# Kernel optimization log

Hardware: AMD Instinct MI355X
Metric: run time of the kernel (lower is better)

Reference implementation:

```python
import jax, jax.numpy as jnp
import numpy as np
import math

N, L, D = 1024, 32, 768
N_OUT, IN_DIM, OUT_DIM = 16, 64, 64
EPS = 1e-8


def setup_inputs() -> dict:
    key = jax.random.key(0)
    ks = jax.random.split(key, 4)
    x = jax.random.normal(ks[0], (N, L, D), jnp.float32)
    mask = jnp.ones((N, L), jnp.float32)
    scaled = lambda k, shape, fan: jax.random.normal(k, shape, jnp.float32) * (1.0 / np.sqrt(fan).astype(np.float32))
    Wscore = scaled(ks[1], (L, D, 1), D)
    Bscore = jnp.zeros((L, 1, 1), jnp.float32)
    Wcap = scaled(ks[2], (L, D, IN_DIM), D)
    Bcap = jnp.zeros((L, 1, IN_DIM), jnp.float32)
    Wvote = scaled(ks[3], (L, N_OUT, IN_DIM, OUT_DIM), IN_DIM)
    Bvote = jnp.zeros((L, N_OUT, 1, OUT_DIM), jnp.float32)
    beta_use = jnp.zeros((L, 1, 1, 1), jnp.float32)
    beta_ign = jnp.zeros((1, N_OUT, 1, 1), jnp.float32)
    return dict(x=x, mask=mask, Wscore=Wscore, Bscore=Bscore, Wcap=Wcap,
                Bcap=Bcap, Wvote=Wvote, Bvote=Bvote, beta_use=beta_use,
                beta_ign=beta_ign, iters=3)


def reference(x, mask, Wscore, Bscore, Wcap, Bcap, Wvote, Bvote, beta_use, beta_ign, iters):
    n_out = Wvote.shape[1]
    half_pi = np.float32(0.5 * math.pi)
    x_t = jnp.transpose(x, (1, 0, 2))                      # [L, N, D]
    a_in = jnp.matmul(x_t, Wscore) + Bscore                # [L, N, 1]
    mu_in = jax.nn.gelu(jnp.matmul(x_t, Wcap) + Bcap, approximate=False)  # [L, N, in_dim]
    f_a_in = jax.nn.sigmoid(a_in) * jnp.transpose(mask)[..., None]        # [L, N, 1]
    f_a_in = f_a_in[:, None, :, :]                         # [L, 1, N, 1]
    # votes: [L, n_out, N, out_dim] (einsum avoids materializing repeated mu_in)
    V = jnp.einsum('lni,lkio->lkno', mu_in, Wvote) + Bvote

    R = jnp.full((1, n_out, 1, 1), 1.0 / n_out, dtype=x.dtype)
    a_out = mu_out = var_out = None
    for t in range(iters):
        if t > 0:
            log_p = (-jnp.sum((V - mu_out[None]) ** 2 / (2.0 * var_out[None] + EPS), axis=-1)
                     - 1.0 - half_pi
                     - 0.5 * jnp.sum(jnp.log(var_out[None] + EPS), axis=-1))   # [L, n_out, N]
            R = jax.nn.softmax(jax.nn.log_sigmoid(a_out)[None] + log_p[..., None], axis=1)
        D_use = f_a_in * R                                  # [L, n_out, N, 1]
        D_ign = f_a_in - D_use
        a_out = jnp.sum(beta_use * D_use, axis=0) - jnp.sum(beta_ign * D_ign, axis=0)  # [n_out, N, 1]
        denom = jnp.sum(D_use, axis=0) + EPS                # [n_out, N, 1]
        mu_out = jnp.sum(D_use * V, axis=0) / denom         # [n_out, N, out_dim]
        var_out = jnp.sum(D_use * (V - mu_out[None]) ** 2, axis=0) / denom

    a_fin = jnp.transpose(a_out[..., 0])                    # [N, n_out]
    mu_fin = jnp.transpose(mu_out, (1, 0, 2))               # [N, n_out, out_dim]
    return a_fin, mu_fin
```

## Files before the change

### kernel.cpp

```cpp
#include <hip/hip_runtime.h>
#include <hip/hip_bf16.h>

#define L_DIM 32
#define N_DIM 1024
#define D_DIM 768
#define K_DIM 16
#define I_DIM 64
#define O_DIM 64
#define EPSF 1e-8f
#define PX 72

typedef unsigned short u16;
typedef __attribute__((ext_vector_type(8))) short short8;
typedef __attribute__((ext_vector_type(4))) float f32x4;
#define MFMA __builtin_amdgcn_mfma_f32_16x16x32_bf16

__device__ __forceinline__ float bf2f(u16 v) {
    union { unsigned int u; float f; } x; x.u = ((unsigned int)v) << 16; return x.f;
}
__device__ __forceinline__ u16 f2bf(float f) {
    union { float f; unsigned int u; } x; x.f = f;
    unsigned int u = x.u;
    u += 0x7FFFu + ((u >> 16) & 1u);
    return (u16)(u >> 16);
}
__device__ __forceinline__ void split2(float v, u16& h, u16& l) {
    u16 hh = f2bf(v);
    h = hh;
    l = f2bf(v - bf2f(hh));
}

__global__ __launch_bounds__(256) void prep_wcap(
    const float* __restrict__ W, u16* __restrict__ H, u16* __restrict__ Lo)
{
    const int l = blockIdx.y, d0 = blockIdx.x * 64, t = threadIdx.x;
    __shared__ float tile[64][65];
    #pragma unroll
    for (int p = 0; p < 4; p++) {
        int dd = p * 16 + (t >> 4), i4 = (t & 15) * 4;
        float4 v = *(const float4*)&W[((size_t)l * D_DIM + d0 + dd) * I_DIM + i4];
        tile[dd][i4] = v.x; tile[dd][i4+1] = v.y; tile[dd][i4+2] = v.z; tile[dd][i4+3] = v.w;
    }
    __syncthreads();
    #pragma unroll
    for (int p = 0; p < 4; p++) {
        int i = p * 16 + (t >> 4), dd0 = (t & 15) * 4;
        u16 h[4], lo[4];
        #pragma unroll
        for (int j = 0; j < 4; j++) split2(tile[dd0 + j][i], h[j], lo[j]);
        size_t base = ((size_t)l * I_DIM + i) * D_DIM + d0 + dd0;
        uint2 ph; ph.x = h[0] | ((unsigned)h[1] << 16); ph.y = h[2] | ((unsigned)h[3] << 16);
        uint2 pl; pl.x = lo[0] | ((unsigned)lo[1] << 16); pl.y = lo[2] | ((unsigned)lo[3] << 16);
        *(uint2*)&H[base] = ph;
        *(uint2*)&Lo[base] = pl;
    }
}

__global__ __launch_bounds__(256) void prep_wvote(
    const float* __restrict__ W, u16* __restrict__ H, u16* __restrict__ Lo)
{
    const int l = blockIdx.y, k = blockIdx.x, t = threadIdx.x;
    __shared__ float tile[64][65];
    #pragma unroll
    for (int p = 0; p < 4; p++) {
        int i = p * 16 + (t >> 4), o4 = (t & 15) * 4;
        float4 v = *(const float4*)&W[(((size_t)l * K_DIM + k) * I_DIM + i) * O_DIM + o4];
        tile[i][o4] = v.x; tile[i][o4+1] = v.y; tile[i][o4+2] = v.z; tile[i][o4+3] = v.w;
    }
    __syncthreads();
    #pragma unroll
    for (int p = 0; p < 4; p++) {
        int o = p * 16 + (t >> 4), i0 = (t & 15) * 4;
        u16 h[4], lo[4];
        #pragma unroll
        for (int j = 0; j < 4; j++) split2(tile[i0 + j][o], h[j], lo[j]);
        size_t base = (((size_t)l * K_DIM + k) * O_DIM + o) * I_DIM + i0;
        uint2 ph; ph.x = h[0] | ((unsigned)h[1] << 16); ph.y = h[2] | ((unsigned)h[3] << 16);
        uint2 pl; pl.x = lo[0] | ((unsigned)lo[1] << 16); pl.y = lo[2] | ((unsigned)lo[3] << 16);
        *(uint2*)&H[base] = ph;
        *(uint2*)&Lo[base] = pl;
    }
}

__global__ __launch_bounds__(256) void kernelA(
    const float* __restrict__ x, const float* __restrict__ mask,
    const float* __restrict__ Wscore, const float* __restrict__ Bscore,
    const u16* __restrict__ WcH, const u16* __restrict__ WcL,
    const float* __restrict__ Bcap,
    float* __restrict__ mu_out, float* __restrict__ fa_out,
    int nbase, int nchunk)
{
    const int l   = blockIdx.y;
    const int n0l = blockIdx.x * 32;
    const int t    = threadIdx.x;
    const int w    = t >> 6;
    const int lane = t & 63;
    const int quad = lane >> 4;
    const int ln16 = lane & 15;

    __shared__ u16 xh[32][PX], xl[32][PX];
    __shared__ float wsc_s[64];
    __shared__ float bcap_s[64];

    if (t < 64) bcap_s[t] = Bcap[l * I_DIM + t];

    f32x4 acc[2] = {{0.f,0.f,0.f,0.f},{0.f,0.f,0.f,0.f}};
    float apart = 0.f;

    for (int ch = 0; ch < 12; ch++) {
        const int k0 = ch * 64;
        __syncthreads();
        #pragma unroll
        for (int p = 0; p < 2; p++) {
            int n = p * 16 + (t >> 4), d0 = (t & 15) * 4;
            float4 v = *(const float4*)&x[((size_t)(nbase + n0l + n) * L_DIM + l) * D_DIM + k0 + d0];
            u16 h[4], lo[4];
            split2(v.x, h[0], lo[0]); split2(v.y, h[1], lo[1]);
            split2(v.z, h[2], lo[2]); split2(v.w, h[3], lo[3]);
            uint2 ph; ph.x = h[0] | ((unsigned)h[1] << 16); ph.y = h[2] | ((unsigned)h[3] << 16);
            uint2 pl; pl.x = lo[0] | ((unsigned)lo[1] << 16); pl.y = lo[2] | ((unsigned)lo[3] << 16);
            *(uint2*)&xh[n][d0] = ph;
            *(uint2*)&xl[n][d0] = pl;
        }
        if (t < 64) wsc_s[t] = Wscore[l * D_DIM + k0 + t];
        __syncthreads();

        {
            const int n = t >> 3, s8 = (t & 7) * 8;
            float ss = 0.f;
            #pragma unroll
            for (int j = 0; j < 8; j++) {
                int dd = s8 + j;
                ss += (bf2f(xh[n][dd]) + bf2f(xl[n][dd])) * wsc_s[dd];
            }
            apart += ss;
        }

        #pragma unroll
        for (int ks = 0; ks < 2; ks++) {
            const int kk = ks * 32;
            size_t wbase = ((size_t)l * I_DIM + (w * 16 + ln16)) * D_DIM + k0 + kk + quad * 8;
            short8 ah = *(const short8*)&WcH[wbase];
            short8 al = *(const short8*)&WcL[wbase];
            #pragma unroll
            for (int c = 0; c < 2; c++) {
                const int n = c * 16 + ln16;
                short8 bh = *(const short8*)&xh[n][kk + quad * 8];
                short8 bl = *(const short8*)&xl[n][kk + quad * 8];
                acc[c] = MFMA(ah, bh, acc[c], 0, 0, 0);
                acc[c] = MFMA(ah, bl, acc[c], 0, 0, 0);
                acc[c] = MFMA(al, bh, acc[c], 0, 0, 0);
            }
        }
    }

    apart += __shfl_xor(apart, 1, 64);
    apart += __shfl_xor(apart, 2, 64);
    apart += __shfl_xor(apart, 4, 64);
    if ((t & 7) == 0) {
        int n = t >> 3;
        float a = apart + Bscore[l];
        float sig = 1.f / (1.f + expf(-a));
        float m = mask[(size_t)(nbase + n0l + n) * L_DIM + l];
        fa_out[(size_t)l * nchunk + n0l + n] = sig * m;
    }

    #pragma unroll
    for (int c = 0; c < 2; c++) {
        const int n = c * 16 + ln16;
        const int i0 = w * 16 + quad * 4;
        float4 o;
        float* op = (float*)&o;
        #pragma unroll
        for (int r = 0; r < 4; r++) {
            float v = acc[c][r] + bcap_s[i0 + r];
            op[r] = 0.5f * v * (1.f + erff(v * 0.70710678118f));
        }
        *(float4*)&mu_out[((size_t)l * nchunk + n0l + n) * I_DIM + i0] = o;
    }
}

__global__ __launch_bounds__(256) void kernelB(
    const float* __restrict__ mu_in,
    const u16* __restrict__ WvH, const u16* __restrict__ WvL,
    const float* __restrict__ Bvote,
    float* __restrict__ V, int nchunk)
{
    const int l   = blockIdx.z;
    const int k   = blockIdx.y;
    const int n0l = blockIdx.x * 64;
    const int t    = threadIdx.x;
    const int w    = t >> 6;
    const int lane = t & 63;
    const int quad = lane >> 4;
    const int ln16 = lane & 15;

    __shared__ u16 mh[64][PX], ml[64][PX];
    __shared__ float bvote_s[64];

    if (t < 64) bvote_s[t] = Bvote[((size_t)l * K_DIM + k) * O_DIM + t];

    #pragma unroll
    for (int p = 0; p < 4; p++) {
        int n = p * 16 + (t >> 4), i0 = (t & 15) * 4;
        float4 v = *(const float4*)&mu_in[((size_t)l * nchunk + n0l + n) * I_DIM + i0];
        u16 h[4], lo[4];
        split2(v.x, h[0], lo[0]); split2(v.y, h[1], lo[1]);
        split2(v.z, h[2], lo[2]); split2(v.w, h[3], lo[3]);
        uint2 ph; ph.x = h[0] | ((unsigned)h[1] << 16); ph.y = h[2] | ((unsigned)h[3] << 16);
        uint2 pl; pl.x = lo[0] | ((unsigned)lo[1] << 16); pl.y = lo[2] | ((unsigned)lo[3] << 16);
        *(uint2*)&mh[n][i0] = ph;
        *(uint2*)&ml[n][i0] = pl;
    }
    __syncthreads();

    f32x4 acc[4] = {{0.f,0.f,0.f,0.f},{0.f,0.f,0.f,0.f},{0.f,0.f,0.f,0.f},{0.f,0.f,0.f,0.f}};

    #pragma unroll
    for (int ks = 0; ks < 2; ks++) {
        const int kk = ks * 32;
        size_t wbase = (((size_t)l * K_DIM + k) * O_DIM + (w * 16 + ln16)) * I_DIM + kk + quad * 8;
        short8 ah = *(const short8*)&WvH[wbase];
        short8 al = *(const short8*)&WvL[wbase];
        #pragma unroll
        for (int c = 0; c < 4; c++) {
            const int n = c * 16 + ln16;
            short8 bh = *(const short8*)&mh[n][kk + quad * 8];
            short8 bl = *(const short8*)&ml[n][kk + quad * 8];
            acc[c] = MFMA(ah, bh, acc[c], 0, 0, 0);
            acc[c] = MFMA(ah, bl, acc[c], 0, 0, 0);
            acc[c] = MFMA(al, bh, acc[c], 0, 0, 0);
        }
    }

    #pragma unroll
    for (int c = 0; c < 4; c++) {
        const int n = c * 16 + ln16;
        const int o0 = w * 16 + quad * 4;
        float4 o;
        o.x = acc[c][0] + bvote_s[o0];
        o.y = acc[c][1] + bvote_s[o0 + 1];
        o.z = acc[c][2] + bvote_s[o0 + 2];
        o.w = acc[c][3] + bvote_s[o0 + 3];
        *(float4*)&V[(((size_t)l * K_DIM + k) * nchunk + n0l + n) * O_DIM + o0] = o;
    }
}

__global__ __launch_bounds__(256) void kernelC(
    const float* __restrict__ V, const float* __restrict__ fa_in,
    const float* __restrict__ beta_use, const float* __restrict__ beta_ign,
    const int* __restrict__ iters_p,
    float* __restrict__ out, int nbase, int nchunk)
{
    const int nl = blockIdx.x;
    const int ng = nbase + nl;
    const int t  = threadIdx.x;
    const int k  = t >> 4;
    const int og = (t & 15) << 2;
    int iters = iters_p[0];
    if (iters < 0 || iters > 16) iters = 3;

    __shared__ float fa_s[32];
    __shared__ float bu_s[32];
    __shared__ float R_s[32][17];
    __shared__ float sc_s[32][17];

    if (t < 32) {
        fa_s[t] = fa_in[(size_t)t * nchunk + nl];
        bu_s[t] = beta_use[t];
    }
    for (int idx = t; idx < 512; idx += 256)
        R_s[idx >> 4][idx & 15] = 1.f / 16.f;
    const float bi_k = beta_ign[k];

    float Vr[32][4];
    #pragma unroll
    for (int l = 0; l < 32; l++) {
        float4 v = *(const float4*)&V[(((size_t)l * K_DIM + k) * nchunk + nl) * O_DIM + og];
        Vr[l][0] = v.x; Vr[l][1] = v.y; Vr[l][2] = v.z; Vr[l][3] = v.w;
    }
    __syncthreads();

    float mu_r[4] = {0.f, 0.f, 0.f, 0.f};
    float var_r[4] = {0.f, 0.f, 0.f, 0.f};
    float a_r = 0.f;

    for (int it = 0; it < iters; it++) {
        if (it > 0) {
            float inv2v[4], lvp = 0.f;
            #pragma unroll
            for (int j = 0; j < 4; j++) {
                inv2v[j] = 1.f / (2.f * var_r[j] + EPSF);
                lvp += logf(var_r[j] + EPSF);
            }
            lvp += __shfl_xor(lvp, 1, 64);
            lvp += __shfl_xor(lvp, 2, 64);
            lvp += __shfl_xor(lvp, 4, 64);
            lvp += __shfl_xor(lvp, 8, 64);
            float ls = fminf(a_r, 0.f) - log1pf(expf(-fabsf(a_r)));
            const float cst = ls - 1.f - 1.57079632679f - 0.5f * lvp;
            #pragma unroll
            for (int l = 0; l < 32; l++) {
                float s = 0.f;
                #pragma unroll
                for (int j = 0; j < 4; j++) {
                    float d = Vr[l][j] - mu_r[j];
                    s += d * d * inv2v[j];
                }
                s = -s;
                s += __shfl_xor(s, 1, 64);
                s += __shfl_xor(s, 2, 64);
                s += __shfl_xor(s, 4, 64);
                s += __shfl_xor(s, 8, 64);
                if ((t & 15) == 0) sc_s[l][k] = s + cst;
            }
            __syncthreads();
            if (t < 32) {
                const int l = t;
                float m = -3.4e38f;
                #pragma unroll
                for (int kk = 0; kk < 16; kk++) m = fmaxf(m, sc_s[l][kk]);
                float e[16]; float sum = 0.f;
                #pragma unroll
                for (int kk = 0; kk < 16; kk++) { e[kk] = expf(sc_s[l][kk] - m); sum += e[kk]; }
                float inv = 1.f / sum;
                #pragma unroll
                for (int kk = 0; kk < 16; kk++) R_s[l][kk] = e[kk] * inv;
            }
            __syncthreads();
        }
        float denom = EPSF, a_acc = 0.f;
        float mu_a[4] = {0.f, 0.f, 0.f, 0.f};
        #pragma unroll
        for (int l = 0; l < 32; l++) {
            float Du = fa_s[l] * R_s[l][k];
            denom += Du;
            #pragma unroll
            for (int j = 0; j < 4; j++) mu_a[j] += Du * Vr[l][j];
            a_acc += bu_s[l] * Du - bi_k * (fa_s[l] - Du);
        }
        float invd = 1.f / denom;
        #pragma unroll
        for (int j = 0; j < 4; j++) mu_r[j] = mu_a[j] * invd;
        a_r = a_acc;
        float var_a[4] = {0.f, 0.f, 0.f, 0.f};
        #pragma unroll
        for (int l = 0; l < 32; l++) {
            float Du = fa_s[l] * R_s[l][k];
            #pragma unroll
            for (int j = 0; j < 4; j++) {
                float d = Vr[l][j] - mu_r[j];
                var_a[j] += Du * d * d;
            }
        }
        #pragma unroll
        for (int j = 0; j < 4; j++) var_r[j] = var_a[j] * invd;
    }

    if ((t & 15) == 0) out[(size_t)ng * K_DIM + k] = a_r;
    float4 o4;
    o4.x = mu_r[0]; o4.y = mu_r[1]; o4.z = mu_r[2]; o4.w = mu_r[3];
    *(float4*)&out[(size_t)N_DIM * K_DIM + ((size_t)ng * K_DIM + k) * O_DIM + og] = o4;
}

extern "C" void kernel_launch(void* const* d_in, const int* in_sizes, int n_in,
                              void* d_out, int out_size, void* d_ws, size_t ws_size,
                              hipStream_t stream) {
    (void)out_size;
    static const int EXP[11] = {25165824, 32768, 24576, 32, 1572864, 64,
                                2097152, 65536, 32, 16, 1};
    int mapi[11];
    bool used[64] = {false};
    for (int s = 0; s < 11; s++) {
        mapi[s] = (s < n_in) ? s : 0;
        for (int j = 0; j < n_in && j < 64; j++) {
            if (!used[j] && in_sizes[j] == EXP[s]) { mapi[s] = j; used[j] = true; break; }
        }
    }
    const float* x        = (const float*)d_in[mapi[0]];
    const float* mask     = (const float*)d_in[mapi[1]];
    const float* Wscore   = (const float*)d_in[mapi[2]];
    const float* Bscore   = (const float*)d_in[mapi[3]];
    const float* Wcap     = (const float*)d_in[mapi[4]];
    const float* Bcap     = (const float*)d_in[mapi[5]];
    const float* Wvote    = (const float*)d_in[mapi[6]];
    const float* Bvote    = (const float*)d_in[mapi[7]];
    const float* beta_use = (const float*)d_in[mapi[8]];
    const float* beta_ign = (const float*)d_in[mapi[9]];
    const int*   iters    = (const int*)d_in[mapi[10]];
    float* out = (float*)d_out;

    const size_t WCAP = (size_t)L_DIM * I_DIM * D_DIM;
    const size_t WVOT = (size_t)L_DIM * K_DIM * O_DIM * I_DIM;
    const size_t WBYTES = 2 * WCAP * 2 + 2 * WVOT * 2;

    int C = 64;
    {
        const int cands[5] = {1024, 512, 256, 128, 64};
        for (int i = 0; i < 5; i++) {
            size_t need = WBYTES + (size_t)cands[i] * (128 + 8192 + 131072);
            if (need <= ws_size) { C = cands[i]; break; }
        }
    }

    char* ws = (char*)d_ws;
    u16* WcH = (u16*)ws;
    u16* WcL = (u16*)(ws + WCAP * 2);
    u16* WvH = (u16*)(ws + WCAP * 4);
    u16* WvL = (u16*)(ws + WCAP * 4 + WVOT * 2);
    char* dyn = ws + WBYTES;
    float* fa = (float*)dyn;
    float* mu = (float*)(dyn + (size_t)128 * C);
    float* V  = (float*)(dyn + (size_t)128 * C + (size_t)8192 * C);

    prep_wcap<<<dim3(12, 32), 256, 0, stream>>>(Wcap, WcH, WcL);
    prep_wvote<<<dim3(16, 32), 256, 0, stream>>>(Wvote, WvH, WvL);

    for (int nbase = 0; nbase < N_DIM; nbase += C) {
        kernelA<<<dim3(C / 32, 32), 256, 0, stream>>>(
            x, mask, Wscore, Bscore, WcH, WcL, Bcap, mu, fa, nbase, C);
        kernelB<<<dim3(C / 64, 16, 32), 256, 0, stream>>>(
            mu, WvH, WvL, Bvote, V, C);
        kernelC<<<dim3(C), 256, 0, stream>>>(
            V, fa, beta_use, beta_ign, iters, out, nbase, C);
    }
}
```

Measured before the change: 297.4 us.

## Make V per-sample contiguous, parallelize softmax, single-pass variance

```diff
diff --git a/kernel.cpp b/kernel.cpp
--- a/kernel.cpp
+++ b/kernel.cpp
@@ -242,7 +242,7 @@
         o.y = acc[c][1] + bvote_s[o0 + 1];
         o.z = acc[c][2] + bvote_s[o0 + 2];
         o.w = acc[c][3] + bvote_s[o0 + 3];
-        *(float4*)&V[(((size_t)l * K_DIM + k) * nchunk + n0l + n) * O_DIM + o0] = o;
+        *(float4*)&V[(((size_t)(n0l + n) * L_DIM + l) * K_DIM + k) * O_DIM + o0] = o;
     }
 }
 
@@ -273,10 +273,11 @@
         R_s[idx >> 4][idx & 15] = 1.f / 16.f;
     const float bi_k = beta_ign[k];
 
+    const float* Vb = V + (size_t)nl * (L_DIM * K_DIM * O_DIM);
     float Vr[32][4];
     #pragma unroll
     for (int l = 0; l < 32; l++) {
-        float4 v = *(const float4*)&V[(((size_t)l * K_DIM + k) * nchunk + nl) * O_DIM + og];
+        float4 v = *(const float4*)&Vb[(l * K_DIM + k) * O_DIM + og];
         Vr[l][0] = v.x; Vr[l][1] = v.y; Vr[l][2] = v.z; Vr[l][3] = v.w;
     }
     __syncthreads();
@@ -315,46 +316,47 @@
                 if ((t & 15) == 0) sc_s[l][k] = s + cst;
             }
             __syncthreads();
-            if (t < 32) {
-                const int l = t;
-                float m = -3.4e38f;
-                #pragma unroll
-                for (int kk = 0; kk < 16; kk++) m = fmaxf(m, sc_s[l][kk]);
-                float e[16]; float sum = 0.f;
-                #pragma unroll
-                for (int kk = 0; kk < 16; kk++) { e[kk] = expf(sc_s[l][kk] - m); sum += e[kk]; }
+            {
+                const int lr = t >> 3;
+                const int c2 = (t & 7) * 2;
+                float s0 = sc_s[lr][c2], s1 = sc_s[lr][c2 + 1];
+                float m = fmaxf(s0, s1);
+                m = fmaxf(m, __shfl_xor(m, 1, 64));
+                m = fmaxf(m, __shfl_xor(m, 2, 64));
+                m = fmaxf(m, __shfl_xor(m, 4, 64));
+                float e0 = expf(s0 - m), e1 = expf(s1 - m);
+                float sum = e0 + e1;
+                sum += __shfl_xor(sum, 1, 64);
+                sum += __shfl_xor(sum, 2, 64);
+                sum += __shfl_xor(sum, 4, 64);
                 float inv = 1.f / sum;
-                #pragma unroll
-                for (int kk = 0; kk < 16; kk++) R_s[l][kk] = e[kk] * inv;
+                R_s[lr][c2]     = e0 * inv;
+                R_s[lr][c2 + 1] = e1 * inv;
             }
             __syncthreads();
         }
         float denom = EPSF, a_acc = 0.f;
         float mu_a[4] = {0.f, 0.f, 0.f, 0.f};
+        float v2_a[4] = {0.f, 0.f, 0.f, 0.f};
         #pragma unroll
         for (int l = 0; l < 32; l++) {
             float Du = fa_s[l] * R_s[l][k];
             denom += Du;
-            #pragma unroll
-            for (int j = 0; j < 4; j++) mu_a[j] += Du * Vr[l][j];
             a_acc += bu_s[l] * Du - bi_k * (fa_s[l] - Du);
-        }
-        float invd = 1.f / denom;
-        #pragma unroll
-        for (int j = 0; j < 4; j++) mu_r[j] = mu_a[j] * invd;
-        a_r = a_acc;
-        float var_a[4] = {0.f, 0.f, 0.f, 0.f};
-        #pragma unroll
-        for (int l = 0; l < 32; l++) {
-            float Du = fa_s[l] * R_s[l][k];
             #pragma unroll
             for (int j = 0; j < 4; j++) {
-                float d = Vr[l][j] - mu_r[j];
-                var_a[j] += Du * d * d;
-            }
-        }
-        #pragma unroll
-        for (int j = 0; j < 4; j++) var_r[j] = var_a[j] * invd;
+                float dv = Du * Vr[l][j];
+                mu_a[j] += dv;
+                v2_a[j] += dv * Vr[l][j];
+            }
+        }
+        float invd = 1.f / denom;
+        #pragma unroll
+        for (int j = 0; j < 4; j++) {
+            mu_r[j] = mu_a[j] * invd;
+            var_r[j] = fmaxf(v2_a[j] * invd - mu_r[j] * mu_r[j], 0.f);
+        }
+        a_r = a_acc;
     }
 
     if ((t & 15) == 0) out[(size_t)ng * K_DIM + k] = a_r;
```

Result: no change. 299.1 us (+0.6%).
